# Performance work log

Hardware: AMD Instinct MI355X
Metric: run time of the kernel (lower is better)

Reference implementation:

```python
import jax, jax.numpy as jnp
import numpy as np

B, T, H, K = 4, 1024, 1024, 16
HD = H // K  # head dim
EPS = 1e-5


def _layernorm(x, g, b):
    mu = jnp.mean(x, axis=-1, keepdims=True)
    var = jnp.mean(jnp.square(x - mu), axis=-1, keepdims=True)
    return (x - mu) * jax.lax.rsqrt(var + EPS) * g + b


def setup_inputs() -> dict:
    key = jax.random.key(0)
    ks = jax.random.split(key, 16)
    s = 0.02
    return {
        "x": jax.random.normal(ks[0], (B, T, H), jnp.float32),
        "ln1_g": jnp.ones((H,), jnp.float32),
        "ln1_b": jnp.zeros((H,), jnp.float32),
        "ln2_g": jnp.ones((H,), jnp.float32),
        "ln2_b": jnp.zeros((H,), jnp.float32),
        "Wq": jax.random.normal(ks[1], (H, H), jnp.float32) * s,
        "bq": jnp.zeros((H,), jnp.float32),
        "Wk": jax.random.normal(ks[2], (H, H), jnp.float32) * s,
        "bk": jnp.zeros((H,), jnp.float32),
        "Wv": jax.random.normal(ks[3], (H, H), jnp.float32) * s,
        "bv": jnp.zeros((H,), jnp.float32),
        "W1": jax.random.normal(ks[4], (H, 4 * H), jnp.float32) * s,
        "b1": jnp.zeros((4 * H,), jnp.float32),
        "W2": jax.random.normal(ks[5], (4 * H, H), jnp.float32) * s,
        "b2": jnp.zeros((H,), jnp.float32),
    }


def reference(x, ln1_g, ln1_b, ln2_g, ln2_b, Wq, bq, Wk, bk, Wv, bv, W1, b1, W2, b2):
    # --- attention sub-block ---
    h = _layernorm(x, ln1_g, ln1_b)                      # (B,T,H)
    q = (h @ Wq + bq).reshape(B, T, K, HD).transpose(0, 2, 1, 3)  # (B,K,T,hd)
    k = (h @ Wk + bk).reshape(B, T, K, HD).transpose(0, 2, 1, 3)
    v = (h @ Wv + bv).reshape(B, T, K, HD).transpose(0, 2, 1, 3)
    qkt = jnp.einsum('bkqd,bkpd->bkqp', q, k)            # (B,K,T,T)
    attn = qkt * (1.0 / np.sqrt(HD))
    # module quirk: masked positions are FILLED with 1e-9 (not -inf) before softmax
    causal_mask = jnp.triu(jnp.ones((T, T), bool), k=1)  # True above diagonal = masked
    attn = jnp.where(causal_mask, jnp.float32(1e-9), attn)
    attn = jax.nn.softmax(attn, axis=-1)
    y = jnp.einsum('bkqp,bkpd->bkqd', attn, v)           # (B,K,T,hd)
    y = y.transpose(0, 2, 1, 3).reshape(B, T, H)
    x = x + y
    # --- MLP sub-block (dropout is identity at eval) ---
    h2 = _layernorm(x, ln2_g, ln2_b)
    m = jax.nn.gelu(h2 @ W1 + b1, approximate=False) @ W2 + b2
    return x + m
```

## Files before the change

kernel.cpp:

```cpp
#include <hip/hip_runtime.h>
#include <hip/hip_bf16.h>
#include <math.h>


typedef __attribute__((ext_vector_type(8))) short bf16x8;
typedef __attribute__((ext_vector_type(4))) float f32x4;

#define DEVINL __device__ __forceinline__

#define LOG2E_SCALE 0.18033688f
#define MASK2 1.4426950408889634e-9f

DEVINL void stage16(const __hip_bfloat16* g, short* l) {
  __builtin_amdgcn_global_load_lds(
      (const __attribute__((address_space(1))) unsigned int*)g,
      (__attribute__((address_space(3))) unsigned int*)l, 16, 0, 0);
}

DEVINL float bf2f(short u) {
  unsigned x = ((unsigned)(unsigned short)u) << 16;
  float f; __builtin_memcpy(&f, &x, 4); return f;
}

DEVINL short f2bf_s(float f) {
  __hip_bfloat16 h = __float2bfloat16(f);
  short s; __builtin_memcpy(&s, &h, 2); return s;
}

DEVINL float block_sum(float v, float* sb) {
  #pragma unroll
  for (int o = 32; o; o >>= 1) v += __shfl_down(v, o);
  const int lane = threadIdx.x & 63, w = threadIdx.x >> 6;
  if (lane == 0) sb[w] = v;
  __syncthreads();
  float r = sb[0] + sb[1] + sb[2] + sb[3];
  __syncthreads();
  return r;
}

template<int BM, int BN, int WM, int WN>
DEVINL void gemm_core64(const __hip_bfloat16* __restrict__ A, int lda,
                        const __hip_bfloat16* __restrict__ Bt, int ldb,
                        int Kd, int row0, int col0,
                        f32x4 (&acc)[WM/16][WN/16],
                        short* lds_a, short* lds_b) {
  constexpr int MI = WM / 16, NI = WN / 16, WNC = BN / WN;
  constexpr int CA = BM * 8, CB = BN * 8;
  const int tid = threadIdx.x;
  const int lane = tid & 63, wave = tid >> 6;
  const int wm = (wave / WNC) * WM, wn = (wave % WNC) * WN;
  const int lr = lane & 15, lq = lane >> 4;
  for (int k0 = 0; k0 < Kd; k0 += 64) {
    #pragma unroll
    for (int c = tid; c < CA; c += 256) {
      const int r = c >> 3, kc = ((c & 7) ^ (r & 7)) << 3;
      stage16(A + (size_t)(row0 + r) * lda + k0 + kc, lds_a + c * 8);
    }
    #pragma unroll
    for (int c = tid; c < CB; c += 256) {
      const int r = c >> 3, kc = ((c & 7) ^ (r & 7)) << 3;
      stage16(Bt + (size_t)(col0 + r) * ldb + k0 + kc, lds_b + c * 8);
    }
    __syncthreads();
    #pragma unroll
    for (int s = 0; s < 2; s++) {
      bf16x8 af[MI], bfr[NI];
      #pragma unroll
      for (int mi = 0; mi < MI; mi++) {
        const int m = wm + mi * 16 + lr;
        af[mi] = *(const bf16x8*)(lds_a + m * 64 + (((s * 4 + lq) ^ (m & 7)) << 3));
      }
      #pragma unroll
      for (int ni = 0; ni < NI; ni++) {
        const int n = wn + ni * 16 + lr;
        bfr[ni] = *(const bf16x8*)(lds_b + n * 64 + (((s * 4 + lq) ^ (n & 7)) << 3));
      }
      #pragma unroll
      for (int mi = 0; mi < MI; mi++)
        #pragma unroll
        for (int ni = 0; ni < NI; ni++)
          acc[mi][ni] = __builtin_amdgcn_mfma_f32_16x16x32_bf16(
              af[mi], bfr[ni], acc[mi][ni], 0, 0, 0);
    }
    __syncthreads();
  }
}

__global__ __launch_bounds__(256) void k_tcvt(const float* __restrict__ src,
                                              __hip_bfloat16* __restrict__ dst,
                                              int R, int C, int dstOff, int dstPitch) {
  __shared__ float tile[32][33];
  const int c0 = blockIdx.x * 32, r0 = blockIdx.y * 32;
  const int tx = threadIdx.x, ty = threadIdx.y;
  #pragma unroll
  for (int i = 0; i < 32; i += 8)
    tile[ty + i][tx] = src[(size_t)(r0 + ty + i) * C + c0 + tx];
  __syncthreads();
  #pragma unroll
  for (int i = 0; i < 32; i += 8)
    dst[(size_t)(c0 + ty + i + dstOff) * dstPitch + r0 + tx] =
        __float2bfloat16(tile[tx][ty + i]);
}

__global__ __launch_bounds__(256) void k_tcvt3(const float* __restrict__ Wq,
                                               const float* __restrict__ Wk,
                                               const float* __restrict__ Wv,
                                               __hip_bfloat16* __restrict__ dst) {
  __shared__ float tile[32][33];
  const float* src = blockIdx.z == 0 ? Wq : (blockIdx.z == 1 ? Wk : Wv);
  const int dstOff = blockIdx.z << 10;
  const int c0 = blockIdx.x * 32, r0 = blockIdx.y * 32;
  const int tx = threadIdx.x, ty = threadIdx.y;
  #pragma unroll
  for (int i = 0; i < 32; i += 8)
    tile[ty + i][tx] = src[(size_t)(r0 + ty + i) * 1024 + c0 + tx];
  __syncthreads();
  #pragma unroll
  for (int i = 0; i < 32; i += 8)
    dst[(size_t)(c0 + ty + i + dstOff) * 1024 + r0 + tx] =
        __float2bfloat16(tile[tx][ty + i]);
}

__global__ __launch_bounds__(256) void k_pack_bias(const float* __restrict__ bq,
                                                   const float* __restrict__ bk,
                                                   const float* __restrict__ bv,
                                                   float* __restrict__ o) {
  const int i = blockIdx.x * 256 + threadIdx.x;
  if (i < 3072)
    o[i] = i < 1024 ? bq[i] : (i < 2048 ? bk[i - 1024] : bv[i - 2048]);
}

__global__ __launch_bounds__(256) void k_ln(const float* __restrict__ x,
                                            const float* __restrict__ y,
                                            const float* __restrict__ g,
                                            const float* __restrict__ bb,
                                            __hip_bfloat16* __restrict__ o,
                                            const float* __restrict__ badd,
                                            float* __restrict__ oinit) {
  __shared__ float sb[4];
  const int t = threadIdx.x;
  const size_t base = (size_t)blockIdx.x * 1024 + t * 4;
  const int c = t * 4;
  float4 xv = *(const float4*)(x + base);
  if (y) {
    float4 yv = *(const float4*)(y + base);
    xv.x += yv.x; xv.y += yv.y; xv.z += yv.z; xv.w += yv.w;
    float4 ov;
    ov.x = xv.x + badd[c + 0]; ov.y = xv.y + badd[c + 1];
    ov.z = xv.z + badd[c + 2]; ov.w = xv.w + badd[c + 3];
    *(float4*)(oinit + base) = ov;
  }
  const float mu = block_sum(xv.x + xv.y + xv.z + xv.w, sb) * (1.f / 1024.f);
  const float dx = xv.x - mu, dy = xv.y - mu, dz = xv.z - mu, dw = xv.w - mu;
  const float var = block_sum(dx * dx + dy * dy + dz * dz + dw * dw, sb) * (1.f / 1024.f);
  const float rs = rsqrtf(var + 1e-5f);
  o[base + 0] = __float2bfloat16(dx * rs * g[c + 0] + bb[c + 0]);
  o[base + 1] = __float2bfloat16(dy * rs * g[c + 1] + bb[c + 1]);
  o[base + 2] = __float2bfloat16(dz * rs * g[c + 2] + bb[c + 2]);
  o[base + 3] = __float2bfloat16(dw * rs * g[c + 3] + bb[c + 3]);
}

__global__ __launch_bounds__(256) void k_gemm_qkv(
    const __hip_bfloat16* __restrict__ h1, const __hip_bfloat16* __restrict__ Wt,
    const float* __restrict__ bqkv, __hip_bfloat16* __restrict__ Q,
    __hip_bfloat16* __restrict__ K, __hip_bfloat16* __restrict__ Vt) {
  __shared__ alignas(16) short smem[16896];
  short* la = smem;
  short* lb = smem + 8192;
  short* lc = smem;
  const int row0 = blockIdx.x * 128, col0 = blockIdx.y * 128;
  f32x4 acc[4][4] = {};
  gemm_core64<128, 128, 64, 64>(h1, 1024, Wt, 1024, 1024, row0, col0, acc, la, lb);
  const int tid = threadIdx.x, lane = tid & 63, wave = tid >> 6;
  const int wm = (wave >> 1) * 64, wn = (wave & 1) * 64, lr = lane & 15, lq = lane >> 4;
  const int which = col0 >> 10;
  const int h0 = (col0 & 1023) >> 6;
  const int b = row0 >> 10, t0 = row0 & 1023;
  if (which < 2) {
    const float qs = (which == 0) ? LOG2E_SCALE : 1.f;
    #pragma unroll
    for (int mi = 0; mi < 4; mi++)
      #pragma unroll
      for (int ni = 0; ni < 4; ni++)
        #pragma unroll
        for (int r = 0; r < 4; r++) {
          const int row = wm + mi * 16 + lq * 4 + r;
          const int col = wn + ni * 16 + lr;
          lc[row * 132 + col] = f2bf_s((acc[mi][ni][r] + bqkv[col0 + col]) * qs);
        }
    __syncthreads();
    __hip_bfloat16* O = which == 0 ? Q : K;
    #pragma unroll
    for (int c = 0; c < 8; c++) {
      const int f = tid + 256 * c;
      const int r = f >> 4, cc = f & 15;
      const int col = cc * 8;
      const int head = h0 + (col >> 6), d = col & 63;
      float4 vv = *(const float4*)(lc + r * 132 + col);
      *(float4*)(O + (((size_t)(b * 16 + head)) << 16) + (t0 + r) * 64 + d) = vv;
    }
  } else {
    #pragma unroll
    for (int mi = 0; mi < 4; mi++)
      #pragma unroll
      for (int ni = 0; ni < 4; ni++)
        #pragma unroll
        for (int r = 0; r < 4; r++) {
          const int row = wm + mi * 16 + lq * 4 + r;
          const int col = wn + ni * 16 + lr;
          lc[col * 132 + row] = f2bf_s(acc[mi][ni][r] + bqkv[col0 + col]);
        }
    __syncthreads();
    #pragma unroll
    for (int c = 0; c < 8; c++) {
      const int f = tid + 256 * c;
      const int dl = f >> 4, tc = f & 15;
      const int head = h0 + (dl >> 6), d = dl & 63;
      float4 vv = *(const float4*)(lc + dl * 132 + tc * 8);
      *(float4*)(Vt + (((size_t)(b * 16 + head)) << 16) + (size_t)d * 1024 +
                 t0 + tc * 8) = vv;
    }
  }
}

__global__ __launch_bounds__(256) void k_tailv(const __hip_bfloat16* __restrict__ Vt,
                                               float* __restrict__ TV) {
  __shared__ float ts[8][64];
  const int hb = blockIdx.x, tid = threadIdx.x;
  const __hip_bfloat16* Vh = Vt + ((size_t)hb << 16);
  for (int w = tid; w < 512; w += 256) {
    const int kt = w >> 6, d = w & 63;
    const short* p = (const short*)(Vh + (size_t)d * 1024 + kt * 128);
    float s = 0.f;
    for (int j = 0; j < 128; j += 8) {
      bf16x8 v = *(const bf16x8*)(p + j);
      #pragma unroll
      for (int e = 0; e < 8; e++) s += bf2f(v[e]);
    }
    ts[kt][d] = s;
  }
  __syncthreads();
  for (int w = tid; w < 512; w += 256) {
    const int qt = w >> 6, d = w & 63;
    float s = 0.f;
    for (int kt = qt + 1; kt < 8; kt++) s += ts[kt][d];
    TV[((size_t)hb * 8 + qt) * 64 + d] = s;
  }
}

__global__ __launch_bounds__(256, 3) void k_attn(
    const __hip_bfloat16* __restrict__ Q, const __hip_bfloat16* __restrict__ K,
    const __hip_bfloat16* __restrict__ Vt, const float* __restrict__ TV,
    float* __restrict__ y) {
  __shared__ short lp[64 * 130];
  __shared__ short lK[128 * 64];
  __shared__ short lV[128 * 64];
  const int hb = blockIdx.y;
  const int j = (blockIdx.y & 32) ? (15 - (int)blockIdx.x) : (int)blockIdx.x;
  const int q0 = j * 64;
  const int nkt = (j >> 1) + 1;
  const int tid = threadIdx.x, lane = tid & 63, wave = tid >> 6;
  const int lr = lane & 15, lq = lane >> 4;
  const int wm = wave * 16;
  const __hip_bfloat16* Qh = Q + ((size_t)hb << 16);
  const __hip_bfloat16* Kh = K + ((size_t)hb << 16);
  const __hip_bfloat16* Vh = Vt + ((size_t)hb << 16);

  bf16x8 qf[2];
  #pragma unroll
  for (int s = 0; s < 2; s++)
    qf[s] = *(const bf16x8*)((const short*)Qh +
                             (size_t)(q0 + wm + lr) * 64 + s * 32 + lq * 8);

  f32x4 oacc[4] = {};
  float mrow[4], lrow[4];
  #pragma unroll
  for (int r = 0; r < 4; r++) { mrow[r] = -1e30f; lrow[r] = 0.f; }

  for (int c = tid; c < 1024; c += 256)
    stage16(Kh + (size_t)(c >> 3) * 64 + (((c & 7) ^ ((c >> 3) & 7)) << 3),
            lK + c * 8);
  __syncthreads();

  for (int kt = 0; kt < nkt; kt++) {
    const int k0 = kt * 128;
    f32x4 sacc[8] = {};
    __builtin_amdgcn_s_setprio(1);
    #pragma unroll
    for (int s = 0; s < 2; s++) {
      bf16x8 bf[8];
      #pragma unroll
      for (int ni = 0; ni < 8; ni++) {
        const int n = ni * 16 + lr;
        bf[ni] = *(const bf16x8*)(lK + n * 64 + (((s * 4 + lq) ^ (n & 7)) << 3));
      }
      #pragma unroll
      for (int ni = 0; ni < 8; ni++)
        sacc[ni] = __builtin_amdgcn_mfma_f32_16x16x32_bf16(
            qf[s], bf[ni], sacc[ni], 0, 0, 0);
    }
    __builtin_amdgcn_s_setprio(0);
    __syncthreads();
    for (int c = tid; c < 1024; c += 256)
      stage16(Vh + (size_t)(c >> 4) * 1024 + k0 + (((c & 15) ^ ((c >> 4) & 15)) << 3),
              lV + c * 8);
    if (kt + 1 < nkt) {
      const int k1 = k0 + 128;
      for (int c = tid; c < 1024; c += 256)
        stage16(Kh + (size_t)(k1 + (c >> 3)) * 64 + (((c & 7) ^ ((c >> 3) & 7)) << 3),
                lK + c * 8);
    }
    const bool last = (kt == nkt - 1);
    #pragma unroll
    for (int r = 0; r < 4; r++) {
      const int grow = q0 + wm + lq * 4 + r;
      float tmax = -1e30f;
      #pragma unroll
      for (int ni = 0; ni < 8; ni++) {
        float v = sacc[ni][r];
        if (last && (k0 + ni * 16 + lr) > grow) v = MASK2;
        sacc[ni][r] = v;
        tmax = fmaxf(tmax, v);
      }
      #pragma unroll
      for (int msk = 8; msk; msk >>= 1) tmax = fmaxf(tmax, __shfl_xor(tmax, msk));
      const float mn = fmaxf(mrow[r], tmax);
      const float al = __builtin_amdgcn_exp2f(mrow[r] - mn);
      float rs = 0.f;
      #pragma unroll
      for (int ni = 0; ni < 8; ni++) {
        const float pv = __builtin_amdgcn_exp2f(sacc[ni][r] - mn);
        sacc[ni][r] = pv;
        rs += pv;
      }
      #pragma unroll
      for (int msk = 8; msk; msk >>= 1) rs += __shfl_xor(rs, msk);
      mrow[r] = mn;
      lrow[r] = lrow[r] * al + rs;
      #pragma unroll
      for (int ni = 0; ni < 4; ni++) oacc[ni][r] *= al;
    }
    #pragma unroll
    for (int r = 0; r < 4; r++) {
      const int row = wm + lq * 4 + r;
      #pragma unroll
      for (int ni = 0; ni < 8; ni++)
        lp[row * 130 + ni * 16 + lr] = f2bf_s(sacc[ni][r]);
    }
    __syncthreads();
    __builtin_amdgcn_s_setprio(1);
    #pragma unroll
    for (int ks = 0; ks < 4; ks++) {
      bf16x8 pa, vb[4];
      pa = *(const bf16x8*)(lp + (wm + lr) * 130 + ks * 32 + lq * 8);
      #pragma unroll
      for (int ni = 0; ni < 4; ni++) {
        const int d = ni * 16 + lr;
        vb[ni] = *(const bf16x8*)(lV + d * 128 + (((ks * 4 + lq) ^ (d & 15)) << 3));
      }
      #pragma unroll
      for (int ni = 0; ni < 4; ni++)
        oacc[ni] = __builtin_amdgcn_mfma_f32_16x16x32_bf16(
            pa, vb[ni], oacc[ni], 0, 0, 0);
    }
    __builtin_amdgcn_s_setprio(0);
  }

  const int b = hb >> 4, h = hb & 15;
  const float cv = (float)(1024 - nkt * 128);
  const float* tv = TV + ((size_t)hb * 8 + (j >> 1)) * 64;
  #pragma unroll
  for (int r = 0; r < 4; r++) {
    const int t = q0 + wm + lq * 4 + r;
    const float tail = __builtin_amdgcn_exp2f(MASK2 - mrow[r]);
    const float inv = 1.f / (lrow[r] + cv * tail);
    #pragma unroll
    for (int ni = 0; ni < 4; ni++) {
      const int d = ni * 16 + lr;
      y[((size_t)(b * 1024 + t) << 10) + h * 64 + d] =
          (oacc[ni][r] + tail * tv[d]) * inv;
    }
  }
}

template<int MH, int NH>
DEVINL void ph_read(const short* pa, const short* pb, int wr, int wc,
                    int lr, int lq, bf16x8 (&af)[4][2], bf16x8 (&bf)[2][2]) {
  if (NH == 0) {
    #pragma unroll
    for (int mi2 = 0; mi2 < 4; mi2++)
      #pragma unroll
      for (int ks = 0; ks < 2; ks++) {
        const int r = wr * 128 + MH * 64 + mi2 * 16 + lr;
        af[mi2][ks] = *(const bf16x8*)(pa + r * 64 + (((ks * 4 + lq) ^ (r & 7)) << 3));
      }
  }
  #pragma unroll
  for (int ni2 = 0; ni2 < 2; ni2++)
    #pragma unroll
    for (int ks = 0; ks < 2; ks++) {
      const int n = wc * 64 + NH * 32 + ni2 * 16 + lr;
      bf[ni2][ks] = *(const bf16x8*)(pb + n * 64 + (((ks * 4 + lq) ^ (n & 7)) << 3));
    }
}

DEVINL void ph_sync() {
  __builtin_amdgcn_s_barrier();
  asm volatile("s_waitcnt lgkmcnt(0)" ::: "memory");
  __builtin_amdgcn_sched_barrier(0);
}

template<int MH, int NH>
DEVINL void ph_mfma(f32x4 (&acc)[8][4], bf16x8 (&af)[4][2], bf16x8 (&bf)[2][2]) {
  __builtin_amdgcn_s_setprio(1);
  #pragma unroll
  for (int mi2 = 0; mi2 < 4; mi2++)
    #pragma unroll
    for (int ni2 = 0; ni2 < 2; ni2++)
      #pragma unroll
      for (int ks = 0; ks < 2; ks++)
        acc[MH * 4 + mi2][NH * 2 + ni2] = __builtin_amdgcn_mfma_f32_16x16x32_bf16(
            af[mi2][ks], bf[ni2][ks], acc[MH * 4 + mi2][NH * 2 + ni2], 0, 0, 0);
  __builtin_amdgcn_s_setprio(0);
  __builtin_amdgcn_s_barrier();
}

__global__ __launch_bounds__(512, 2) void k_gemm_mlp1(const __hip_bfloat16* __restrict__ h2,
                                                      const __hip_bfloat16* __restrict__ W1t,
                                                      const float* __restrict__ b1,
                                                      __hip_bfloat16* __restrict__ G) {
  __shared__ alignas(16) short smem[65536];
  short* Ae = smem;
  short* Ao = smem + 16384;
  short* Be = smem + 32768;
  short* Bo = smem + 49152;
  const int row0 = blockIdx.x * 256, col0 = blockIdx.y * 256;
  const int tid = threadIdx.x, lane = tid & 63, wid = tid >> 6;
  const int lr = lane & 15, lq = lane >> 4;
  const int wr = wid >> 2, wc = wid & 3;
  const __hip_bfloat16* A = h2 + (size_t)row0 * 1024;
  const __hip_bfloat16* Bt = W1t + (size_t)col0 * 1024;

  auto STG = [&](const __hip_bfloat16* src, int k0, int h, short* dst, int SH) {
    #pragma unroll
    for (int ii = 0; ii < 2; ii++) {
      const int f = tid + ii * 512;
      const int rp = f >> 3, P = f & 7;
      const int r = ((rp >> SH) << (SH + 1)) | (h << SH) | (rp & ((1 << SH) - 1));
      const int g = P ^ (r & 7);
      stage16(src + (size_t)r * 1024 + k0 + g * 8, dst + r * 64 + P * 8);
    }
  };

  f32x4 acc[8][4] = {};
  bf16x8 af[4][2], bf[2][2];

  STG(A, 0, 0, Ae, 6);  STG(Bt, 0, 0, Be, 5);
  STG(A, 0, 1, Ae, 6);  STG(Bt, 0, 1, Be, 5);
  STG(A, 64, 0, Ao, 6); STG(Bt, 64, 0, Bo, 5);
  asm volatile("s_waitcnt vmcnt(4)" ::: "memory");
  __syncthreads();

  for (int i = 0; i < 8; ++i) {
    const int kE1 = (i + 1) * 128;
    const int kO0 = i * 128 + 64;
    const int kO1 = kE1 + 64;
    const bool more = (i + 1 < 8);
    ph_read<0, 0>(Ae, Be, wr, wc, lr, lq, af, bf);
    STG(A, kO0, 1, Ao, 6);
    ph_sync();
    ph_mfma<0, 0>(acc, af, bf);
    ph_read<0, 1>(Ae, Be, wr, wc, lr, lq, af, bf);
    STG(Bt, kO0, 1, Bo, 5);
    ph_sync();
    ph_mfma<0, 1>(acc, af, bf);
    ph_read<1, 0>(Ae, Be, wr, wc, lr, lq, af, bf);
    if (more) STG(A, kE1, 0, Ae, 6);
    ph_sync();
    ph_mfma<1, 0>(acc, af, bf);
    ph_read<1, 1>(Ae, Be, wr, wc, lr, lq, af, bf);
    if (more) {
      STG(Bt, kE1, 0, Be, 5);
      asm volatile("s_waitcnt vmcnt(4)" ::: "memory");
    } else {
      asm volatile("s_waitcnt vmcnt(0)" ::: "memory");
    }
    ph_sync();
    ph_mfma<1, 1>(acc, af, bf);
    ph_read<0, 0>(Ao, Bo, wr, wc, lr, lq, af, bf);
    if (more) STG(A, kE1, 1, Ae, 6);
    ph_sync();
    ph_mfma<0, 0>(acc, af, bf);
    ph_read<0, 1>(Ao, Bo, wr, wc, lr, lq, af, bf);
    if (more) STG(Bt, kE1, 1, Be, 5);
    ph_sync();
    ph_mfma<0, 1>(acc, af, bf);
    ph_read<1, 0>(Ao, Bo, wr, wc, lr, lq, af, bf);
    if (more) STG(A, kO1, 0, Ao, 6);
    ph_sync();
    ph_mfma<1, 0>(acc, af, bf);
    ph_read<1, 1>(Ao, Bo, wr, wc, lr, lq, af, bf);
    if (more) {
      STG(Bt, kO1, 0, Bo, 5);
      asm volatile("s_waitcnt vmcnt(4)" ::: "memory");
    }
    ph_sync();
    ph_mfma<1, 1>(acc, af, bf);
  }

  short* lc = smem;
  #pragma unroll
  for (int pr = 0; pr < 4; pr++) {
    if ((wid >> 2) == (pr >> 1)) {
      const int mib = (pr & 1) * 4;
      #pragma unroll
      for (int mi2 = 0; mi2 < 4; mi2++)
        #pragma unroll
        for (int ni = 0; ni < 4; ni++)
          #pragma unroll
          for (int rr = 0; rr < 4; rr++) {
            const int rloc = mi2 * 16 + lq * 4 + rr;
            const int col = (wid & 3) * 64 + ni * 16 + lr;
            float v = acc[mib + mi2][ni][rr] + b1[col0 + col];
            const float u2 = fminf(v * (2.3022079f + 0.1029434f * v * v), 80.f);
            const float e = __builtin_amdgcn_exp2f(u2);
            v = v * e * __builtin_amdgcn_rcpf(e + 1.f);
            lc[rloc * 264 + col] = f2bf_s(v);
          }
    }
    __syncthreads();
    #pragma unroll
    for (int c = 0; c < 4; c++) {
      const int f = tid + 512 * c;
      const int r = f >> 5, cc = f & 31;
      float4 vv = *(const float4*)(lc + r * 264 + cc * 8);
      *(float4*)(G + ((size_t)(row0 + pr * 64 + r) << 12) + col0 + cc * 8) = vv;
    }
    __syncthreads();
  }
}

template<int MH>
DEVINL void mmh(f32x4 (&acc)[4][2], bf16x8 (&af)[2][2], bf16x8 (&bf)[2][2]) {
  __builtin_amdgcn_s_setprio(1);
  #pragma unroll
  for (int mi2 = 0; mi2 < 2; mi2++)
    #pragma unroll
    for (int ni = 0; ni < 2; ni++)
      #pragma unroll
      for (int ks = 0; ks < 2; ks++)
        acc[MH * 2 + mi2][ni] = __builtin_amdgcn_mfma_f32_16x16x32_bf16(
            af[mi2][ks], bf[ni][ks], acc[MH * 2 + mi2][ni], 0, 0, 0);
  __builtin_amdgcn_s_setprio(0);
  __builtin_amdgcn_s_barrier();
}

__global__ __launch_bounds__(512, 2) void k_gemm_mlp2(const __hip_bfloat16* __restrict__ G,
                                                      const __hip_bfloat16* __restrict__ W2t,
                                                      float* __restrict__ out) {
  __shared__ alignas(16) short smem[32768];
  short* Ae = smem;
  short* Ao = smem + 8192;
  short* Be = smem + 16384;
  short* Bo = smem + 24576;
  const int row0 = blockIdx.x * 128, col0 = blockIdx.y * 128;
  const int tid = threadIdx.x, lane = tid & 63, wid = tid >> 6;
  const int lr = lane & 15, lq = lane >> 4;
  const int wr = wid >> 2, wc = wid & 3;
  const __hip_bfloat16* A = G + (size_t)row0 * 4096;
  const __hip_bfloat16* Bt = W2t + (size_t)col0 * 4096;

  auto STGA = [&](int k0, int h, short* dst) {
    const int rp = tid >> 3, P = tid & 7;
    const int r = ((rp >> 5) << 6) | (h << 5) | (rp & 31);
    const int g = P ^ (r & 7);
    stage16(A + (size_t)r * 4096 + k0 + g * 8, dst + r * 64 + P * 8);
  };
  auto STGB = [&](int k0, short* dst) {
    #pragma unroll
    for (int ii = 0; ii < 2; ii++) {
      const int f = tid + ii * 512;
      const int r = f >> 3, P = f & 7;
      const int g = P ^ (r & 7);
      stage16(Bt + (size_t)r * 4096 + k0 + g * 8, dst + r * 64 + P * 8);
    }
  };

  f32x4 acc[4][2] = {};
  bf16x8 af[2][2], bf[2][2];

  auto RDA = [&](const short* pa, int MH) {
    #pragma unroll
    for (int mi2 = 0; mi2 < 2; mi2++)
      #pragma unroll
      for (int ks = 0; ks < 2; ks++) {
        const int r = wr * 64 + MH * 32 + mi2 * 16 + lr;
        af[mi2][ks] = *(const bf16x8*)(pa + r * 64 + (((ks * 4 + lq) ^ (r & 7)) << 3));
      }
  };
  auto RDB = [&](const short* pb) {
    #pragma unroll
    for (int ni = 0; ni < 2; ni++)
      #pragma unroll
      for (int ks = 0; ks < 2; ks++) {
        const int n = wc * 32 + ni * 16 + lr;
        bf[ni][ks] = *(const bf16x8*)(pb + n * 64 + (((ks * 4 + lq) ^ (n & 7)) << 3));
      }
  };

  STGB(0, Be); STGA(0, 0, Ae);
  STGA(0, 1, Ae);
  STGB(64, Bo); STGA(64, 0, Ao);
  asm volatile("s_waitcnt vmcnt(4)" ::: "memory");
  __syncthreads();

  for (int i = 0; i < 32; ++i) {
    const int kE1 = (i + 1) * 128, kO0 = i * 128 + 64, kO1 = kE1 + 64;
    const bool more = (i + 1 < 32);
    RDA(Ae, 0); RDB(Be);
    STGA(kO0, 1, Ao);
    asm volatile("s_waitcnt vmcnt(4)" ::: "memory");
    ph_sync();
    mmh<0>(acc, af, bf);
    RDA(Ae, 1);
    if (more) {
      STGB(kE1, Be); STGA(kE1, 0, Ae);
      asm volatile("s_waitcnt vmcnt(4)" ::: "memory");
    } else {
      asm volatile("s_waitcnt vmcnt(1)" ::: "memory");
    }
    ph_sync();
    mmh<1>(acc, af, bf);
    RDA(Ao, 0); RDB(Bo);
    if (more) {
      STGA(kE1, 1, Ae);
      asm volatile("s_waitcnt vmcnt(4)" ::: "memory");
    } else {
      asm volatile("s_waitcnt vmcnt(0)" ::: "memory");
    }
    ph_sync();
    mmh<0>(acc, af, bf);
    RDA(Ao, 1);
    if (more) {
      STGB(kO1, Bo); STGA(kO1, 0, Ao);
      asm volatile("s_waitcnt vmcnt(4)" ::: "memory");
    }
    ph_sync();
    mmh<1>(acc, af, bf);
  }

  #pragma unroll
  for (int mi = 0; mi < 4; mi++)
    #pragma unroll
    for (int ni = 0; ni < 2; ni++)
      #pragma unroll
      for (int rr = 0; rr < 4; rr++) {
        const int grow = row0 + wr * 64 + (mi >> 1) * 32 + (mi & 1) * 16 + lq * 4 + rr;
        const int gcol = col0 + wc * 32 + ni * 16 + lr;
        float* p = out + (((size_t)grow << 10) + gcol);
        *p += acc[mi][ni][rr];
      }
}

extern "C" void kernel_launch(void* const* d_in, const int* in_sizes, int n_in,
                              void* d_out, int out_size, void* d_ws, size_t ws_size,
                              hipStream_t stream) {
  const float* x     = (const float*)d_in[0];
  const float* ln1_g = (const float*)d_in[1];
  const float* ln1_b = (const float*)d_in[2];
  const float* ln2_g = (const float*)d_in[3];
  const float* ln2_b = (const float*)d_in[4];
  const float* Wq    = (const float*)d_in[5];
  const float* bq    = (const float*)d_in[6];
  const float* Wk    = (const float*)d_in[7];
  const float* bk    = (const float*)d_in[8];
  const float* Wv    = (const float*)d_in[9];
  const float* bv    = (const float*)d_in[10];
  const float* W1    = (const float*)d_in[11];
  const float* b1    = (const float*)d_in[12];
  const float* W2    = (const float*)d_in[13];
  const float* b2    = (const float*)d_in[14];
  float* out = (float*)d_out;

  char* p = (char*)d_ws;
  auto alloc = [&](size_t bytes) { char* r = p; p += (bytes + 255) & ~(size_t)255; return r; };
  __hip_bfloat16* wqkv = (__hip_bfloat16*)alloc(3072 * 1024 * 2);
  __hip_bfloat16* w1t  = (__hip_bfloat16*)alloc(4096 * 1024 * 2);
  __hip_bfloat16* w2t  = (__hip_bfloat16*)alloc(1024 * 4096 * 2);
  float*          bqkv = (float*)alloc(3072 * 4);
  __hip_bfloat16* h1   = (__hip_bfloat16*)alloc(4096 * 1024 * 2);
  __hip_bfloat16* Qb   = (__hip_bfloat16*)alloc((size_t)64 * 65536 * 2);
  __hip_bfloat16* Kb   = (__hip_bfloat16*)alloc((size_t)64 * 65536 * 2);
  __hip_bfloat16* Vt   = (__hip_bfloat16*)alloc((size_t)64 * 65536 * 2);
  float*          TV   = (float*)alloc((size_t)64 * 8 * 64 * 4);
  float*          yb   = (float*)alloc((size_t)4096 * 1024 * 4);
  __hip_bfloat16* h2   = (__hip_bfloat16*)alloc(4096 * 1024 * 2);
  __hip_bfloat16* G    = (__hip_bfloat16*)alloc((size_t)4096 * 4096 * 2);
  (void)ws_size; (void)in_sizes; (void)n_in; (void)out_size;

  const dim3 b256(256), bt(32, 8);
  k_tcvt3<<<dim3(32, 32, 3), bt, 0, stream>>>(Wq, Wk, Wv, wqkv);
  k_tcvt<<<dim3(128, 32), bt, 0, stream>>>(W1, w1t, 1024, 4096, 0, 1024);
  k_tcvt<<<dim3(32, 128), bt, 0, stream>>>(W2, w2t, 4096, 1024, 0, 4096);
  k_pack_bias<<<12, b256, 0, stream>>>(bq, bk, bv, bqkv);

  k_ln<<<4096, b256, 0, stream>>>(x, nullptr, ln1_g, ln1_b, h1, nullptr, nullptr);
  k_gemm_qkv<<<dim3(32, 24), b256, 0, stream>>>(h1, wqkv, bqkv, Qb, Kb, Vt);
  k_tailv<<<64, b256, 0, stream>>>(Vt, TV);
  k_attn<<<dim3(16, 64), b256, 0, stream>>>(Qb, Kb, Vt, TV, yb);

  k_ln<<<4096, b256, 0, stream>>>(x, yb, ln2_g, ln2_b, h2, b2, out);
  k_gemm_mlp1<<<dim3(16, 16), dim3(512), 0, stream>>>(h2, w1t, b1, G);
  k_gemm_mlp2<<<dim3(32, 8), dim3(512), 0, stream>>>(G, w2t, out);
}
```

Measured before the change: 307.6 us.

## Rewrite QKV GEMM as 8-wave double-buffered pipelined kernel

Replaces the simple single-buffered gemm_core64 in the QKV projection with the 512-thread, double-buffered, phase-interleaved pipeline already used by the MLP2 kernel. Global-to-LDS staging for the next k-slices overlaps MFMA work, using explicit vmcnt waits, barriers and setprio. The aim is to hide load latency and raise MFMA utilisation for this GEMM. In exchange it uses twice the LDS and more barriers, and correctness depends on hand-tuned waitcnt counts.

Measured after the change: 304.5 us. No clear change (-1.0%).

```diff
diff --git a/kernel.cpp b/kernel.cpp
--- a/kernel.cpp
+++ b/kernel.cpp
@@ -38,52 +38,61 @@
   return r;
 }
 
-template<int BM, int BN, int WM, int WN>
-DEVINL void gemm_core64(const __hip_bfloat16* __restrict__ A, int lda,
-                        const __hip_bfloat16* __restrict__ Bt, int ldb,
-                        int Kd, int row0, int col0,
-                        f32x4 (&acc)[WM/16][WN/16],
-                        short* lds_a, short* lds_b) {
-  constexpr int MI = WM / 16, NI = WN / 16, WNC = BN / WN;
-  constexpr int CA = BM * 8, CB = BN * 8;
-  const int tid = threadIdx.x;
-  const int lane = tid & 63, wave = tid >> 6;
-  const int wm = (wave / WNC) * WM, wn = (wave % WNC) * WN;
-  const int lr = lane & 15, lq = lane >> 4;
-  for (int k0 = 0; k0 < Kd; k0 += 64) {
-    #pragma unroll
-    for (int c = tid; c < CA; c += 256) {
-      const int r = c >> 3, kc = ((c & 7) ^ (r & 7)) << 3;
-      stage16(A + (size_t)(row0 + r) * lda + k0 + kc, lds_a + c * 8);
-    }
-    #pragma unroll
-    for (int c = tid; c < CB; c += 256) {
-      const int r = c >> 3, kc = ((c & 7) ^ (r & 7)) << 3;
-      stage16(Bt + (size_t)(col0 + r) * ldb + k0 + kc, lds_b + c * 8);
-    }
-    __syncthreads();
-    #pragma unroll
-    for (int s = 0; s < 2; s++) {
-      bf16x8 af[MI], bfr[NI];
-      #pragma unroll
-      for (int mi = 0; mi < MI; mi++) {
-        const int m = wm + mi * 16 + lr;
-        af[mi] = *(const bf16x8*)(lds_a + m * 64 + (((s * 4 + lq) ^ (m & 7)) << 3));
-      }
-      #pragma unroll
-      for (int ni = 0; ni < NI; ni++) {
-        const int n = wn + ni * 16 + lr;
-        bfr[ni] = *(const bf16x8*)(lds_b + n * 64 + (((s * 4 + lq) ^ (n & 7)) << 3));
-      }
-      #pragma unroll
-      for (int mi = 0; mi < MI; mi++)
-        #pragma unroll
-        for (int ni = 0; ni < NI; ni++)
-          acc[mi][ni] = __builtin_amdgcn_mfma_f32_16x16x32_bf16(
-              af[mi], bfr[ni], acc[mi][ni], 0, 0, 0);
-    }
-    __syncthreads();
-  }
+DEVINL void ph_sync() {
+  __builtin_amdgcn_s_barrier();
+  asm volatile("s_waitcnt lgkmcnt(0)" ::: "memory");
+  __builtin_amdgcn_sched_barrier(0);
+}
+
+template<int MH>
+DEVINL void mmh(f32x4 (&acc)[4][2], bf16x8 (&af)[2][2], bf16x8 (&bf)[2][2]) {
+  __builtin_amdgcn_s_setprio(1);
+  #pragma unroll
+  for (int mi2 = 0; mi2 < 2; mi2++)
+    #pragma unroll
+    for (int ni = 0; ni < 2; ni++)
+      #pragma unroll
+      for (int ks = 0; ks < 2; ks++)
+        acc[MH * 2 + mi2][ni] = __builtin_amdgcn_mfma_f32_16x16x32_bf16(
+            af[mi2][ks], bf[ni][ks], acc[MH * 2 + mi2][ni], 0, 0, 0);
+  __builtin_amdgcn_s_setprio(0);
+  __builtin_amdgcn_s_barrier();
+}
+
+template<int MH, int NH>
+DEVINL void ph_read(const short* pa, const short* pb, int wr, int wc,
+                    int lr, int lq, bf16x8 (&af)[4][2], bf16x8 (&bf)[2][2]) {
+  if (NH == 0) {
+    #pragma unroll
+    for (int mi2 = 0; mi2 < 4; mi2++)
+      #pragma unroll
+      for (int ks = 0; ks < 2; ks++) {
+        const int r = wr * 128 + MH * 64 + mi2 * 16 + lr;
+        af[mi2][ks] = *(const bf16x8*)(pa + r * 64 + (((ks * 4 + lq) ^ (r & 7)) << 3));
+      }
+  }
+  #pragma unroll
+  for (int ni2 = 0; ni2 < 2; ni2++)
+    #pragma unroll
+    for (int ks = 0; ks < 2; ks++) {
+      const int n = wc * 64 + NH * 32 + ni2 * 16 + lr;
+      bf[ni2][ks] = *(const bf16x8*)(pb + n * 64 + (((ks * 4 + lq) ^ (n & 7)) << 3));
+    }
+}
+
+template<int MH, int NH>
+DEVINL void ph_mfma(f32x4 (&acc)[8][4], bf16x8 (&af)[4][2], bf16x8 (&bf)[2][2]) {
+  __builtin_amdgcn_s_setprio(1);
+  #pragma unroll
+  for (int mi2 = 0; mi2 < 4; mi2++)
+    #pragma unroll
+    for (int ni2 = 0; ni2 < 2; ni2++)
+      #pragma unroll
+      for (int ks = 0; ks < 2; ks++)
+        acc[MH * 4 + mi2][NH * 2 + ni2] = __builtin_amdgcn_mfma_f32_16x16x32_bf16(
+            af[mi2][ks], bf[ni2][ks], acc[MH * 4 + mi2][NH * 2 + ni2], 0, 0, 0);
+  __builtin_amdgcn_s_setprio(0);
+  __builtin_amdgcn_s_barrier();
 }
 
 __global__ __launch_bounds__(256) void k_tcvt(const float* __restrict__ src,
@@ -160,39 +169,122 @@
   o[base + 3] = __float2bfloat16(dw * rs * g[c + 3] + bb[c + 3]);
 }
 
-__global__ __launch_bounds__(256) void k_gemm_qkv(
+__global__ __launch_bounds__(512, 2) void k_gemm_qkv(
     const __hip_bfloat16* __restrict__ h1, const __hip_bfloat16* __restrict__ Wt,
     const float* __restrict__ bqkv, __hip_bfloat16* __restrict__ Q,
     __hip_bfloat16* __restrict__ K, __hip_bfloat16* __restrict__ Vt) {
-  __shared__ alignas(16) short smem[16896];
-  short* la = smem;
-  short* lb = smem + 8192;
-  short* lc = smem;
+  __shared__ alignas(16) short smem[32768];
+  short* Ae = smem;
+  short* Ao = smem + 8192;
+  short* Be = smem + 16384;
+  short* Bo = smem + 24576;
   const int row0 = blockIdx.x * 128, col0 = blockIdx.y * 128;
-  f32x4 acc[4][4] = {};
-  gemm_core64<128, 128, 64, 64>(h1, 1024, Wt, 1024, 1024, row0, col0, acc, la, lb);
-  const int tid = threadIdx.x, lane = tid & 63, wave = tid >> 6;
-  const int wm = (wave >> 1) * 64, wn = (wave & 1) * 64, lr = lane & 15, lq = lane >> 4;
+  const int tid = threadIdx.x, lane = tid & 63, wid = tid >> 6;
+  const int lr = lane & 15, lq = lane >> 4;
+  const int wr = wid >> 2, wc = wid & 3;
+  const __hip_bfloat16* A = h1 + (size_t)row0 * 1024;
+  const __hip_bfloat16* Bt = Wt + (size_t)col0 * 1024;
+
+  auto STGA = [&](int k0, int h, short* dst) {
+    const int rp = tid >> 3, P = tid & 7;
+    const int r = ((rp >> 5) << 6) | (h << 5) | (rp & 31);
+    const int g = P ^ (r & 7);
+    stage16(A + (size_t)r * 1024 + k0 + g * 8, dst + r * 64 + P * 8);
+  };
+  auto STGB = [&](int k0, short* dst) {
+    #pragma unroll
+    for (int ii = 0; ii < 2; ii++) {
+      const int f = tid + ii * 512;
+      const int r = f >> 3, P = f & 7;
+      const int g = P ^ (r & 7);
+      stage16(Bt + (size_t)r * 1024 + k0 + g * 8, dst + r * 64 + P * 8);
+    }
+  };
+
+  f32x4 acc[4][2] = {};
+  bf16x8 af[2][2], bf[2][2];
+
+  auto RDA = [&](const short* pa, int MH) {
+    #pragma unroll
+    for (int mi2 = 0; mi2 < 2; mi2++)
+      #pragma unroll
+      for (int ks = 0; ks < 2; ks++) {
+        const int r = wr * 64 + MH * 32 + mi2 * 16 + lr;
+        af[mi2][ks] = *(const bf16x8*)(pa + r * 64 + (((ks * 4 + lq) ^ (r & 7)) << 3));
+      }
+  };
+  auto RDB = [&](const short* pb) {
+    #pragma unroll
+    for (int ni = 0; ni < 2; ni++)
+      #pragma unroll
+      for (int ks = 0; ks < 2; ks++) {
+        const int n = wc * 32 + ni * 16 + lr;
+        bf[ni][ks] = *(const bf16x8*)(pb + n * 64 + (((ks * 4 + lq) ^ (n & 7)) << 3));
+      }
+  };
+
+  STGB(0, Be); STGA(0, 0, Ae);
+  STGA(0, 1, Ae);
+  STGB(64, Bo); STGA(64, 0, Ao);
+  asm volatile("s_waitcnt vmcnt(4)" ::: "memory");
+  __syncthreads();
+
+  for (int i = 0; i < 8; ++i) {
+    const int kE1 = (i + 1) * 128, kO0 = i * 128 + 64, kO1 = kE1 + 64;
+    const bool more = (i + 1 < 8);
+    RDA(Ae, 0); RDB(Be);
+    STGA(kO0, 1, Ao);
+    asm volatile("s_waitcnt vmcnt(4)" ::: "memory");
+    ph_sync();
+    mmh<0>(acc, af, bf);
+    RDA(Ae, 1);
+    if (more) {
+      STGB(kE1, Be); STGA(kE1, 0, Ae);
+      asm volatile("s_waitcnt vmcnt(4)" ::: "memory");
+    } else {
+      asm volatile("s_waitcnt vmcnt(1)" ::: "memory");
+    }
+    ph_sync();
+    mmh<1>(acc, af, bf);
+    RDA(Ao, 0); RDB(Bo);
+    if (more) {
+      STGA(kE1, 1, Ae);
+      asm volatile("s_waitcnt vmcnt(4)" ::: "memory");
+    } else {
+      asm volatile("s_waitcnt vmcnt(0)" ::: "memory");
+    }
+    ph_sync();
+    mmh<0>(acc, af, bf);
+    RDA(Ao, 1);
+    if (more) {
+      STGB(kO1, Bo); STGA(kO1, 0, Ao);
+      asm volatile("s_waitcnt vmcnt(4)" ::: "memory");
+    }
+    ph_sync();
+    mmh<1>(acc, af, bf);
+  }
+
   const int which = col0 >> 10;
   const int h0 = (col0 & 1023) >> 6;
   const int b = row0 >> 10, t0 = row0 & 1023;
+  short* lc = smem;
   if (which < 2) {
     const float qs = (which == 0) ? LOG2E_SCALE : 1.f;
     #pragma unroll
     for (int mi = 0; mi < 4; mi++)
       #pragma unroll
-      for (int ni = 0; ni < 4; ni++)
+      for (int ni = 0; ni < 2; ni++)
         #pragma unroll
-        for (int r = 0; r < 4; r++) {
-          const int row = wm + mi * 16 + lq * 4 + r;
-          const int col = wn + ni * 16 + lr;
-          lc[row * 132 + col] = f2bf_s((acc[mi][ni][r] + bqkv[col0 + col]) * qs);
+        for (int rr = 0; rr < 4; rr++) {
+          const int row = wr * 64 + (mi >> 1) * 32 + (mi & 1) * 16 + lq * 4 + rr;
+          const int col = wc * 32 + ni * 16 + lr;
+          lc[row * 132 + col] = f2bf_s((acc[mi][ni][rr] + bqkv[col0 + col]) * qs);
         }
     __syncthreads();
     __hip_bfloat16* O = which == 0 ? Q : K;
     #pragma unroll
-    for (int c = 0; c < 8; c++) {
-      const int f = tid + 256 * c;
+    for (int c = 0; c < 4; c++) {
+      const int f = tid + 512 * c;
       const int r = f >> 4, cc = f & 15;
       const int col = cc * 8;
       const int head = h0 + (col >> 6), d = col & 63;
@@ -203,17 +295,17 @@
     #pragma unroll
     for (int mi = 0; mi < 4; mi++)
       #pragma unroll
-      for (int ni = 0; ni < 4; ni++)
+      for (int ni = 0; ni < 2; ni++)
         #pragma unroll
-        for (int r = 0; r < 4; r++) {
-          const int row = wm + mi * 16 + lq * 4 + r;
-          const int col = wn + ni * 16 + lr;
-          lc[col * 132 + row] = f2bf_s(acc[mi][ni][r] + bqkv[col0 + col]);
+        for (int rr = 0; rr < 4; rr++) {
+          const int row = wr * 64 + (mi >> 1) * 32 + (mi & 1) * 16 + lq * 4 + rr;
+          const int col = wc * 32 + ni * 16 + lr;
+          lc[col * 132 + row] = f2bf_s(acc[mi][ni][rr] + bqkv[col0 + col]);
         }
     __syncthreads();
     #pragma unroll
-    for (int c = 0; c < 8; c++) {
-      const int f = tid + 256 * c;
+    for (int c = 0; c < 4; c++) {
+      const int f = tid + 512 * c;
       const int dl = f >> 4, tc = f & 15;
       const int head = h0 + (dl >> 6), d = dl & 63;
       float4 vv = *(const float4*)(lc + dl * 132 + tc * 8);
@@ -383,48 +475,6 @@
   }
 }
 
-template<int MH, int NH>
-DEVINL void ph_read(const short* pa, const short* pb, int wr, int wc,
-                    int lr, int lq, bf16x8 (&af)[4][2], bf16x8 (&bf)[2][2]) {
-  if (NH == 0) {
-    #pragma unroll
-    for (int mi2 = 0; mi2 < 4; mi2++)
-      #pragma unroll
-      for (int ks = 0; ks < 2; ks++) {
-        const int r = wr * 128 + MH * 64 + mi2 * 16 + lr;
-        af[mi2][ks] = *(const bf16x8*)(pa + r * 64 + (((ks * 4 + lq) ^ (r & 7)) << 3));
-      }
-  }
-  #pragma unroll
-  for (int ni2 = 0; ni2 < 2; ni2++)
-    #pragma unroll
-    for (int ks = 0; ks < 2; ks++) {
-      const int n = wc * 64 + NH * 32 + ni2 * 16 + lr;
-      bf[ni2][ks] = *(const bf16x8*)(pb + n * 64 + (((ks * 4 + lq) ^ (n & 7)) << 3));
-    }
-}
-
-DEVINL void ph_sync() {
-  __builtin_amdgcn_s_barrier();
-  asm volatile("s_waitcnt lgkmcnt(0)" ::: "memory");
-  __builtin_amdgcn_sched_barrier(0);
-}
-
-template<int MH, int NH>
-DEVINL void ph_mfma(f32x4 (&acc)[8][4], bf16x8 (&af)[4][2], bf16x8 (&bf)[2][2]) {
-  __builtin_amdgcn_s_setprio(1);
-  #pragma unroll
-  for (int mi2 = 0; mi2 < 4; mi2++)
-    #pragma unroll
-    for (int ni2 = 0; ni2 < 2; ni2++)
-      #pragma unroll
-      for (int ks = 0; ks < 2; ks++)
-        acc[MH * 4 + mi2][NH * 2 + ni2] = __builtin_amdgcn_mfma_f32_16x16x32_bf16(
-            af[mi2][ks], bf[ni2][ks], acc[MH * 4 + mi2][NH * 2 + ni2], 0, 0, 0);
-  __builtin_amdgcn_s_setprio(0);
-  __builtin_amdgcn_s_barrier();
-}
-
 __global__ __launch_bounds__(512, 2) void k_gemm_mlp1(const __hip_bfloat16* __restrict__ h2,
                                                       const __hip_bfloat16* __restrict__ W1t,
                                                       const float* __restrict__ b1,
@@ -538,21 +588,6 @@
     }
     __syncthreads();
   }
-}
-
-template<int MH>
-DEVINL void mmh(f32x4 (&acc)[4][2], bf16x8 (&af)[2][2], bf16x8 (&bf)[2][2]) {
-  __builtin_amdgcn_s_setprio(1);
-  #pragma unroll
-  for (int mi2 = 0; mi2 < 2; mi2++)
-    #pragma unroll
-    for (int ni = 0; ni < 2; ni++)
-      #pragma unroll
-      for (int ks = 0; ks < 2; ks++)
-        acc[MH * 2 + mi2][ni] = __builtin_amdgcn_mfma_f32_16x16x32_bf16(
-            af[mi2][ks], bf[ni][ks], acc[MH * 2 + mi2][ni], 0, 0, 0);
-  __builtin_amdgcn_s_setprio(0);
-  __builtin_amdgcn_s_barrier();
 }
 
 __global__ __launch_bounds__(512, 2) void k_gemm_mlp2(const __hip_bfloat16* __restrict__ G,
@@ -705,7 +740,7 @@
   k_pack_bias<<<12, b256, 0, stream>>>(bq, bk, bv, bqkv);
 
   k_ln<<<4096, b256, 0, stream>>>(x, nullptr, ln1_g, ln1_b, h1, nullptr, nullptr);
-  k_gemm_qkv<<<dim3(32, 24), b256, 0, stream>>>(h1, wqkv, bqkv, Qb, Kb, Vt);
+  k_gemm_qkv<<<dim3(32, 24), dim3(512), 0, stream>>>(h1, wqkv, bqkv, Qb, Kb, Vt);
   k_tailv<<<64, b256, 0, stream>>>(Vt, TV);
   k_attn<<<dim3(16, 64), b256, 0, stream>>>(Qb, Kb, Vt, TV, yb);
 
```
